# Kernel tuning notes

Hardware: AMD Instinct MI355X
Metric: run time of the kernel (lower is better)

The kernel has to match this reference:

```python
import jax, jax.numpy as jnp
import numpy as np

N_NODES = 50000
N_EDGES = 800000
D = 128


def setup_inputs() -> dict:
    key = jax.random.key(0)
    k1, k2, k3, k4 = jax.random.split(key, 4)
    x = jax.random.normal(k1, (N_NODES, D), dtype=jnp.float32)
    # nn.Linear(in, out, bias=False) weight: [out, in]
    W = jax.random.normal(k2, (D, D), dtype=jnp.float32) / np.sqrt(D)
    src = jax.random.randint(k3, (N_EDGES,), 0, N_NODES, dtype=jnp.int64)
    dst = jax.random.randint(k4, (N_EDGES,), 0, N_NODES, dtype=jnp.int64)
    return {"x": x, "W": W, "src": src, "dst": dst}


def reference(x, W, src, dst):
    # copy_src + reduce_sum: sum incoming neighbor features per destination node
    agg = jax.ops.segment_sum(x[src], dst, num_segments=N_NODES)  # [N, D]
    h = agg @ W.T                      # linear, no bias
    h = jax.nn.relu(h)                 # dropout is identity in eval mode
    h = h + x                          # residual (is_normalize=False)
    return h
```

## Files before the change

### kernel.cpp

```cpp
#include <hip/hip_runtime.h>

#define N_NODES 50000
#define N_EDGES 800000
#define D 128

#define P1_BLOCKS 128
#define P1_GRID   1024
#define EDGES_PER_BLOCK (N_EDGES / P1_BLOCKS)
#define N_BINS 782
#define CHUNK_CAP 31
#define CELL_WORDS 32
#define LIST_CAP 48
#define RS 136

#define WS_WB16   0
#define WS_SORTED 8192
#define WS_XBF16  3211264
#define WS_END_SORT ((size_t)(WS_XBF16 + 3200000) * 4)

#define NB_SCAN ((N_NODES + 255) / 256)
#define WS_CNT     0
#define WS_ROWPTR  50000
#define WS_BSUMS   100352
#define WS_SRCS    100608
#define WS_END_CSR ((size_t)(WS_SRCS + N_EDGES) * 4)

using bf16x8 = __attribute__((ext_vector_type(8))) short;
using f32x4  = __attribute__((ext_vector_type(4))) float;

__device__ __forceinline__ unsigned bf16rne(float f) {
    unsigned b = __float_as_uint(f);
    return (b + 0x7fffu + ((b >> 16) & 1u)) >> 16;
}

__device__ __forceinline__ uint4 pack8(float4 a, float4 b) {
    uint4 o;
    o.x = bf16rne(a.x) | (bf16rne(a.y) << 16);
    o.y = bf16rne(a.z) | (bf16rne(a.w) << 16);
    o.z = bf16rne(b.x) | (bf16rne(b.y) << 16);
    o.w = bf16rne(b.z) | (bf16rne(b.w) << 16);
    return o;
}

__global__ __launch_bounds__(256) void p1_convert_partition_kernel(
    const float* __restrict__ x, const float* __restrict__ W,
    const int* __restrict__ src, const int* __restrict__ dst,
    uint4* __restrict__ xb, uint4* __restrict__ wb,
    unsigned* __restrict__ sorted)
{
    const int tid = threadIdx.x;

    if (blockIdx.x >= P1_BLOCKS) {
        const int cb = blockIdx.x - P1_BLOCKS;
        const int gid = cb * 256 + tid;
        const int stride = (P1_GRID - P1_BLOCKS) * 256;
        const float4* x4 = (const float4*)x;
        for (int i = gid; i < (N_NODES * D) / 8; i += stride)
            xb[i] = pack8(x4[2 * i], x4[2 * i + 1]);
        const float4* W4 = (const float4*)W;
        for (int i = gid; i < (D * D) / 8; i += stride)
            wb[i] = pack8(W4[2 * i], W4[2 * i + 1]);
        return;
    }

    __shared__ int lhist[N_BINS];
    for (int b = tid; b < N_BINS; b += 256) lhist[b] = 0;
    __syncthreads();
    const int e0 = blockIdx.x * EDGES_PER_BLOCK;
    for (int i = tid; i < EDGES_PER_BLOCK; i += 256) {
        int e = e0 + i;
        int d = dst[e];
        int bin = d >> 6;
        int pos = atomicAdd(&lhist[bin], 1);
        if (pos < CHUNK_CAP)
            sorted[(size_t)(bin * P1_BLOCKS + blockIdx.x) * CELL_WORDS + 1 + pos] =
                ((unsigned)(d & 63) << 16) | ((unsigned)src[e] & 0xffffu);
    }
    __syncthreads();
    for (int b = tid; b < N_BINS; b += 256)
        sorted[(size_t)(b * P1_BLOCKS + blockIdx.x) * CELL_WORDS] = (unsigned)lhist[b];
}

__device__ __forceinline__ void acc_u4(float* acc, uint4 v)
{
    acc[0] += __uint_as_float(v.x << 16);
    acc[1] += __uint_as_float(v.x & 0xffff0000u);
    acc[2] += __uint_as_float(v.y << 16);
    acc[3] += __uint_as_float(v.y & 0xffff0000u);
    acc[4] += __uint_as_float(v.z << 16);
    acc[5] += __uint_as_float(v.z & 0xffff0000u);
    acc[6] += __uint_as_float(v.w << 16);
    acc[7] += __uint_as_float(v.w & 0xffff0000u);
}

__global__ __launch_bounds__(1024) void gather_gemm_kernel(
    const uint4* __restrict__ xb, const unsigned* __restrict__ sorted,
    const unsigned short* __restrict__ Wb, float* __restrict__ out)
{
    __shared__ unsigned short list[64 * LIST_CAP];
    __shared__ int lcnt[64];
    __shared__ unsigned short Ab[64 * RS];
    const int tid = threadIdx.x;
    const int bin = blockIdx.x;
    if (tid < 64) lcnt[tid] = 0;
    __syncthreads();

    {
        const int ch = tid >> 3;
        const int sub = tid & 7;
        const unsigned* base = sorted + (size_t)(bin * P1_BLOCKS + ch) * CELL_WORDS;
        int cc = (int)base[0];
        if (cc > CHUNK_CAP) cc = CHUNK_CAP;
        for (int i = sub; i < cc; i += 8) {
            unsigned p = base[1 + i];
            int dl = p >> 16;
            int pos = atomicAdd(&lcnt[dl], 1);
            if (pos < LIST_CAP) list[dl * LIST_CAP + pos] = (unsigned short)(p & 0xffffu);
        }
    }
    __syncthreads();

    {
        const int nl = tid >> 4;
        const int lane = tid & 15;
        int cc = lcnt[nl];
        if (cc > LIST_CAP) cc = LIST_CAP;
        const unsigned short* bk = &list[nl * LIST_CAP];

        float acc[8];
        #pragma unroll
        for (int i = 0; i < 8; ++i) acc[i] = 0.f;
        int e = 0;
        for (; e + 8 <= cc; e += 8) {
            uint4 v[8];
            #pragma unroll
            for (int j = 0; j < 8; ++j) v[j] = xb[(int)bk[e + j] * 16 + lane];
            #pragma unroll
            for (int j = 0; j < 8; ++j) acc_u4(acc, v[j]);
        }
        for (; e + 4 <= cc; e += 4) {
            uint4 v0 = xb[(int)bk[e] * 16 + lane];
            uint4 v1 = xb[(int)bk[e + 1] * 16 + lane];
            uint4 v2 = xb[(int)bk[e + 2] * 16 + lane];
            uint4 v3 = xb[(int)bk[e + 3] * 16 + lane];
            acc_u4(acc, v0); acc_u4(acc, v1); acc_u4(acc, v2); acc_u4(acc, v3);
        }
        for (; e < cc; ++e) acc_u4(acc, xb[(int)bk[e] * 16 + lane]);

        unsigned short* arow = &Ab[nl * RS + lane * 8];
        #pragma unroll
        for (int i = 0; i < 8; ++i) arow[i] = (unsigned short)bf16rne(acc[i]);
    }
    __syncthreads();

    const int wv = tid >> 6;
    const int lane64 = tid & 63;
    const int m = lane64 & 15;
    const int quad = lane64 >> 4;
    const int rt = wv >> 2;

    bf16x8 afrag[4];
    #pragma unroll
    for (int s = 0; s < 4; ++s)
        afrag[s] = *(const bf16x8*)(&Ab[(rt * 16 + m) * RS + quad * 8 + s * 32]);

    const unsigned short* xbs = (const unsigned short*)xb;

    #pragma unroll
    for (int half = 0; half < 2; ++half) {
        const int ct = (wv & 3) * 2 + half;
        f32x4 acc = {0.f, 0.f, 0.f, 0.f};
        const unsigned short* wrow = Wb + (size_t)(ct * 16 + m) * D + quad * 8;
        #pragma unroll
        for (int s = 0; s < 4; ++s) {
            bf16x8 bfrag = *(const bf16x8*)(wrow + s * 32);
            acc = __builtin_amdgcn_mfma_f32_16x16x32_bf16(afrag[s], bfrag, acc, 0, 0, 0);
        }
        const int cc2 = ct * 16 + m;
        #pragma unroll
        for (int r = 0; r < 4; ++r) {
            int rr = bin * 64 + rt * 16 + quad * 4 + r;
            if (rr < N_NODES) {
                float xf = __uint_as_float((unsigned)xbs[(size_t)rr * D + cc2] << 16);
                out[(size_t)rr * D + cc2] = fmaxf(acc[r], 0.f) + xf;
            }
        }
    }
}

__global__ __launch_bounds__(256) void hist_kernel(
    const int* __restrict__ dst, int* __restrict__ cnt)
{
    int e = blockIdx.x * 256 + threadIdx.x;
    if (e < N_EDGES) atomicAdd(&cnt[dst[e]], 1);
}

__device__ __forceinline__ int block_excl_scan_256(int v, int* wsums)
{
    const int lane = threadIdx.x & 63;
    const int wid = threadIdx.x >> 6;
    int incl = v;
    #pragma unroll
    for (int off = 1; off < 64; off <<= 1) {
        int t = __shfl_up(incl, off, 64);
        if (lane >= off) incl += t;
    }
    if (lane == 63) wsums[wid] = incl;
    __syncthreads();
    if (threadIdx.x == 0) {
        int s = 0;
        #pragma unroll
        for (int w = 0; w < 4; ++w) { int t = wsums[w]; wsums[w] = s; s += t; }
    }
    __syncthreads();
    return wsums[wid] + incl - v;
}

__global__ __launch_bounds__(256) void scan_reduce_kernel(
    const int* __restrict__ cnt, int* __restrict__ bsums)
{
    __shared__ int wsums[4];
    int i = blockIdx.x * 256 + threadIdx.x;
    int v = (i < N_NODES) ? cnt[i] : 0;
    const int lane = threadIdx.x & 63;
    int s = v;
    #pragma unroll
    for (int off = 32; off >= 1; off >>= 1) s += __shfl_down(s, off, 64);
    if (lane == 0) wsums[threadIdx.x >> 6] = s;
    __syncthreads();
    if (threadIdx.x == 0)
        bsums[blockIdx.x] = wsums[0] + wsums[1] + wsums[2] + wsums[3];
}

__global__ __launch_bounds__(256) void scan_bsums_kernel(
    int* __restrict__ bsums, int* __restrict__ row_ptr)
{
    __shared__ int wsums[4];
    int t = threadIdx.x;
    int v = (t < NB_SCAN) ? bsums[t] : 0;
    int excl = block_excl_scan_256(v, wsums);
    if (t < NB_SCAN) bsums[t] = excl;
    if (t == 255) row_ptr[N_NODES] = excl + v;
}

__global__ __launch_bounds__(256) void scan_final_kernel(
    int* __restrict__ cnt, const int* __restrict__ bsums,
    int* __restrict__ row_ptr)
{
    __shared__ int wsums[4];
    int i = blockIdx.x * 256 + threadIdx.x;
    int v = (i < N_NODES) ? cnt[i] : 0;
    int excl = block_excl_scan_256(v, wsums) + bsums[blockIdx.x];
    if (i < N_NODES) { row_ptr[i] = excl; cnt[i] = excl; }
}

__global__ __launch_bounds__(256) void csr_scatter_kernel(
    const int* __restrict__ src, const int* __restrict__ dst,
    int* __restrict__ cursor, int* __restrict__ srcs)
{
    int e = blockIdx.x * 256 + threadIdx.x;
    if (e < N_EDGES) {
        int pos = atomicAdd(&cursor[dst[e]], 1);
        srcs[pos] = src[e];
    }
}

__global__ __launch_bounds__(256) void gather_kernel(
    const float* __restrict__ x, const int* __restrict__ row_ptr,
    const int* __restrict__ srcs, float* __restrict__ agg)
{
    int gid = blockIdx.x * 256 + threadIdx.x;
    int node = gid >> 5;
    int lane = gid & 31;
    if (node >= N_NODES) return;
    int e = row_ptr[node];
    const int e_end = row_ptr[node + 1];
    const float4* x4 = (const float4*)x;
    float4 acc = make_float4(0.f, 0.f, 0.f, 0.f);
    for (; e + 4 <= e_end; e += 4) {
        int s0 = srcs[e], s1 = srcs[e + 1], s2 = srcs[e + 2], s3 = srcs[e + 3];
        float4 v0 = x4[(size_t)s0 * 32 + lane];
        float4 v1 = x4[(size_t)s1 * 32 + lane];
        float4 v2 = x4[(size_t)s2 * 32 + lane];
        float4 v3 = x4[(size_t)s3 * 32 + lane];
        acc.x += (v0.x + v1.x) + (v2.x + v3.x);
        acc.y += (v0.y + v1.y) + (v2.y + v3.y);
        acc.z += (v0.z + v1.z) + (v2.z + v3.z);
        acc.w += (v0.w + v1.w) + (v2.w + v3.w);
    }
    for (; e < e_end; ++e) {
        float4 v = x4[(size_t)srcs[e] * 32 + lane];
        acc.x += v.x; acc.y += v.y; acc.z += v.z; acc.w += v.w;
    }
    ((float4*)agg)[(size_t)node * 32 + lane] = acc;
}

__global__ __launch_bounds__(256) void scatter_add_kernel(
    const float* __restrict__ x, const int* __restrict__ src,
    const int* __restrict__ dst, float* __restrict__ agg)
{
    int gid = blockIdx.x * 256 + threadIdx.x;
    int edge = gid >> 5;
    int lane = gid & 31;
    if (edge >= N_EDGES) return;
    int s = src[edge];
    int d = dst[edge];
    const float4 v = *(const float4*)(x + (size_t)s * D + lane * 4);
    float* a = agg + (size_t)d * D + lane * 4;
    atomicAdd(a + 0, v.x);
    atomicAdd(a + 1, v.y);
    atomicAdd(a + 2, v.z);
    atomicAdd(a + 3, v.w);
}

#define G_ROWS 64

__global__ __launch_bounds__(256) void gemm_relu_res_kernel(
    float* __restrict__ agg, const float* __restrict__ W,
    const float* __restrict__ x)
{
    __shared__ float Wl[64 * 128];
    __shared__ float Al[G_ROWS * 128];

    const int tid = threadIdx.x;
    const int row0 = blockIdx.x * G_ROWS;

    for (int i = tid; i < G_ROWS * 32; i += 256) {
        int r = i >> 5;
        int c4 = (i & 31) << 2;
        int gr = row0 + r;
        float4 v = make_float4(0.f, 0.f, 0.f, 0.f);
        if (gr < N_NODES) v = *(const float4*)(agg + (size_t)gr * D + c4);
        *(float4*)(Al + r * 128 + c4) = v;
    }

    const int cg = tid & 31;
    const int rg = tid >> 5;
    const int c0 = cg << 2;
    const int r0 = rg << 3;

    float acc[8][4];
    #pragma unroll
    for (int i = 0; i < 8; ++i)
        #pragma unroll
        for (int j = 0; j < 4; ++j) acc[i][j] = 0.f;

    for (int h = 0; h < 2; ++h) {
        __syncthreads();
        for (int i = tid; i < 64 * 128; i += 256) {
            int c = i >> 6, kk = i & 63;
            int c_swz = (((c >> 2) ^ (kk & 31)) << 2) | (c & 3);
            Wl[kk * 128 + c_swz] = W[c * 128 + h * 64 + kk];
        }
        __syncthreads();

        for (int kc = 0; kc < 64; kc += 4) {
            float a[8][4];
            #pragma unroll
            for (int i = 0; i < 8; ++i) {
                float4 t = *(const float4*)(&Al[(r0 + i) * 128 + h * 64 + kc]);
                a[i][0] = t.x; a[i][1] = t.y; a[i][2] = t.z; a[i][3] = t.w;
            }
            #pragma unroll
            for (int j = 0; j < 4; ++j) {
                int kk = kc + j;
                const float4 wv =
                    *(const float4*)(&Wl[kk * 128 + ((cg ^ (kk & 31)) << 2)]);
                #pragma unroll
                for (int i = 0; i < 8; ++i) {
                    acc[i][0] = fmaf(a[i][j], wv.x, acc[i][0]);
                    acc[i][1] = fmaf(a[i][j], wv.y, acc[i][1]);
                    acc[i][2] = fmaf(a[i][j], wv.z, acc[i][2]);
                    acc[i][3] = fmaf(a[i][j], wv.w, acc[i][3]);
                }
            }
        }
    }

    #pragma unroll
    for (int i = 0; i < 8; ++i) {
        int gr = row0 + r0 + i;
        if (gr >= N_NODES) continue;
        const float4 xv = *(const float4*)(x + (size_t)gr * D + c0);
        float4 o;
        o.x = fmaxf(acc[i][0], 0.f) + xv.x;
        o.y = fmaxf(acc[i][1], 0.f) + xv.y;
        o.z = fmaxf(acc[i][2], 0.f) + xv.z;
        o.w = fmaxf(acc[i][3], 0.f) + xv.w;
        *(float4*)(agg + (size_t)gr * D + c0) = o;
    }
}

extern "C" void kernel_launch(void* const* d_in, const int* in_sizes, int n_in,
                              void* d_out, int out_size, void* d_ws, size_t ws_size,
                              hipStream_t stream) {
    const float* x  = (const float*)d_in[0];
    const float* W  = (const float*)d_in[1];
    const int*  src = (const int*)d_in[2];
    const int*  dst = (const int*)d_in[3];
    float* agg = (float*)d_out;

    const int eb = (N_EDGES + 255) / 256;
    int* ws = (int*)d_ws;

    if (ws_size >= WS_END_SORT) {
        uint4*    wb     = (uint4*)(ws + WS_WB16);
        unsigned* sorted = (unsigned*)(ws + WS_SORTED);
        uint4*    xb     = (uint4*)(ws + WS_XBF16);

        p1_convert_partition_kernel<<<P1_GRID, 256, 0, stream>>>(
            x, W, src, dst, xb, wb, sorted);
        gather_gemm_kernel<<<N_BINS, 1024, 0, stream>>>(
            xb, sorted, (const unsigned short*)wb, (float*)d_out);
    } else if (ws_size >= WS_END_CSR) {
        int* cnt     = ws + WS_CNT;
        int* row_ptr = ws + WS_ROWPTR;
        int* bsums   = ws + WS_BSUMS;
        int* srcs    = ws + WS_SRCS;

        hipMemsetAsync(cnt, 0, (size_t)N_NODES * sizeof(int), stream);
        hist_kernel<<<eb, 256, 0, stream>>>(dst, cnt);
        scan_reduce_kernel<<<NB_SCAN, 256, 0, stream>>>(cnt, bsums);
        scan_bsums_kernel<<<1, 256, 0, stream>>>(bsums, row_ptr);
        scan_final_kernel<<<NB_SCAN, 256, 0, stream>>>(cnt, bsums, row_ptr);
        csr_scatter_kernel<<<eb, 256, 0, stream>>>(src, dst, cnt, srcs);
        int total = N_NODES * 32;
        gather_kernel<<<(total + 255) / 256, 256, 0, stream>>>(x, row_ptr, srcs, agg);
        gemm_relu_res_kernel<<<(N_NODES + G_ROWS - 1) / G_ROWS, 256, 0, stream>>>(agg, W, x);
    } else {
        hipMemsetAsync(agg, 0, (size_t)N_NODES * D * sizeof(float), stream);
        int total = N_EDGES * 32;
        scatter_add_kernel<<<(total + 255) / 256, 256, 0, stream>>>(x, src, dst, agg);
        gemm_relu_res_kernel<<<(N_NODES + G_ROWS - 1) / G_ROWS, 256, 0, stream>>>(agg, W, x);
    }
}
```

Measured before the change: 159.7 us.

## Fuse partition/convert and gather-GEMM into one cooperative kernel with grid sync

Combines the edge-partition/bf16-conversion kernel and the gather+MFMA GEMM kernel into a single cooperative launch of 512 blocks of 1024 threads. A grid-wide sync separates the phases, and the second phase loops over bins with a grid stride. The aim is to remove the second kernel launch and the inter-kernel gap. In exchange, each phase runs on fewer threads than before (128 partition blocks at 1024 threads, and 512 blocks for 782 bins, so some blocks handle two bins). A grid sync is added, and if the cooperative launch fails the code falls back to the old two-kernel path.

```diff
diff --git a/kernel.cpp b/kernel.cpp
--- a/kernel.cpp
+++ b/kernel.cpp
@@ -1,4 +1,7 @@
 #include <hip/hip_runtime.h>
+#include <hip/hip_cooperative_groups.h>
+
+namespace cg = cooperative_groups;
 
 #define N_NODES 50000
 #define N_EDGES 800000
@@ -6,6 +9,7 @@
 
 #define P1_BLOCKS 128
 #define P1_GRID   1024
+#define FUSED_GRID 512
 #define EDGES_PER_BLOCK (N_EDGES / P1_BLOCKS)
 #define N_BINS 782
 #define CHUNK_CAP 31
@@ -40,6 +44,150 @@
     o.z = bf16rne(b.x) | (bf16rne(b.y) << 16);
     o.w = bf16rne(b.z) | (bf16rne(b.w) << 16);
     return o;
+}
+
+__device__ __forceinline__ void acc_u4(float* acc, uint4 v)
+{
+    acc[0] += __uint_as_float(v.x << 16);
+    acc[1] += __uint_as_float(v.x & 0xffff0000u);
+    acc[2] += __uint_as_float(v.y << 16);
+    acc[3] += __uint_as_float(v.y & 0xffff0000u);
+    acc[4] += __uint_as_float(v.z << 16);
+    acc[5] += __uint_as_float(v.z & 0xffff0000u);
+    acc[6] += __uint_as_float(v.w << 16);
+    acc[7] += __uint_as_float(v.w & 0xffff0000u);
+}
+
+__global__ __launch_bounds__(1024, 8) void fused_gcn_kernel(
+    const float* __restrict__ x, const float* __restrict__ W,
+    const int* __restrict__ src, const int* __restrict__ dst,
+    uint4* __restrict__ xb, uint4* __restrict__ wb,
+    unsigned* __restrict__ sorted, float* __restrict__ out)
+{
+    __shared__ int lhist[N_BINS];
+    __shared__ unsigned short list[64 * LIST_CAP];
+    __shared__ int lcnt[64];
+    __shared__ unsigned short Ab[64 * RS];
+    const int tid = threadIdx.x;
+    const int bid = blockIdx.x;
+
+    if (bid < P1_BLOCKS) {
+        for (int b = tid; b < N_BINS; b += 1024) lhist[b] = 0;
+        __syncthreads();
+        const int e0 = bid * EDGES_PER_BLOCK;
+        for (int i = tid; i < EDGES_PER_BLOCK; i += 1024) {
+            int e = e0 + i;
+            int d = dst[e];
+            int bin = d >> 6;
+            int pos = atomicAdd(&lhist[bin], 1);
+            if (pos < CHUNK_CAP)
+                sorted[(size_t)(bin * P1_BLOCKS + bid) * CELL_WORDS + 1 + pos] =
+                    ((unsigned)(d & 63) << 16) | ((unsigned)src[e] & 0xffffu);
+        }
+        __syncthreads();
+        for (int b = tid; b < N_BINS; b += 1024)
+            sorted[(size_t)(b * P1_BLOCKS + bid) * CELL_WORDS] = (unsigned)lhist[b];
+    } else {
+        const int gid = (bid - P1_BLOCKS) * 1024 + tid;
+        const int stride = (FUSED_GRID - P1_BLOCKS) * 1024;
+        const float4* x4 = (const float4*)x;
+        for (int i = gid; i < (N_NODES * D) / 8; i += stride)
+            xb[i] = pack8(x4[2 * i], x4[2 * i + 1]);
+        const float4* W4 = (const float4*)W;
+        for (int i = gid; i < (D * D) / 8; i += stride)
+            wb[i] = pack8(W4[2 * i], W4[2 * i + 1]);
+    }
+
+    __threadfence();
+    cg::this_grid().sync();
+
+    const unsigned short* Wb  = (const unsigned short*)wb;
+    const unsigned short* xbs = (const unsigned short*)xb;
+
+    for (int bin = bid; bin < N_BINS; bin += FUSED_GRID) {
+        if (tid < 64) lcnt[tid] = 0;
+        __syncthreads();
+
+        {
+            const int ch = tid >> 3;
+            const int sub = tid & 7;
+            const unsigned* base = sorted + (size_t)(bin * P1_BLOCKS + ch) * CELL_WORDS;
+            int cc = (int)base[0];
+            if (cc > CHUNK_CAP) cc = CHUNK_CAP;
+            for (int i = sub; i < cc; i += 8) {
+                unsigned p = base[1 + i];
+                int dl = p >> 16;
+                int pos = atomicAdd(&lcnt[dl], 1);
+                if (pos < LIST_CAP) list[dl * LIST_CAP + pos] = (unsigned short)(p & 0xffffu);
+            }
+        }
+        __syncthreads();
+
+        {
+            const int nl = tid >> 4;
+            const int lane = tid & 15;
+            int cc = lcnt[nl];
+            if (cc > LIST_CAP) cc = LIST_CAP;
+            const unsigned short* bk = &list[nl * LIST_CAP];
+
+            float acc[8];
+            #pragma unroll
+            for (int i = 0; i < 8; ++i) acc[i] = 0.f;
+            int e = 0;
+            for (; e + 8 <= cc; e += 8) {
+                uint4 v[8];
+                #pragma unroll
+                for (int j = 0; j < 8; ++j) v[j] = xb[(int)bk[e + j] * 16 + lane];
+                #pragma unroll
+                for (int j = 0; j < 8; ++j) acc_u4(acc, v[j]);
+            }
+            for (; e + 4 <= cc; e += 4) {
+                uint4 v0 = xb[(int)bk[e] * 16 + lane];
+                uint4 v1 = xb[(int)bk[e + 1] * 16 + lane];
+                uint4 v2 = xb[(int)bk[e + 2] * 16 + lane];
+                uint4 v3 = xb[(int)bk[e + 3] * 16 + lane];
+                acc_u4(acc, v0); acc_u4(acc, v1); acc_u4(acc, v2); acc_u4(acc, v3);
+            }
+            for (; e < cc; ++e) acc_u4(acc, xb[(int)bk[e] * 16 + lane]);
+
+            unsigned short* arow = &Ab[nl * RS + lane * 8];
+            #pragma unroll
+            for (int i = 0; i < 8; ++i) arow[i] = (unsigned short)bf16rne(acc[i]);
+        }
+        __syncthreads();
+
+        const int wv = tid >> 6;
+        const int lane64 = tid & 63;
+        const int m = lane64 & 15;
+        const int quad = lane64 >> 4;
+        const int rt = wv >> 2;
+
+        bf16x8 afrag[4];
+        #pragma unroll
+        for (int s = 0; s < 4; ++s)
+            afrag[s] = *(const bf16x8*)(&Ab[(rt * 16 + m) * RS + quad * 8 + s * 32]);
+
+        #pragma unroll
+        for (int half = 0; half < 2; ++half) {
+            const int ct = (wv & 3) * 2 + half;
+            f32x4 acc = {0.f, 0.f, 0.f, 0.f};
+            const unsigned short* wrow = Wb + (size_t)(ct * 16 + m) * D + quad * 8;
+            #pragma unroll
+            for (int s = 0; s < 4; ++s) {
+                bf16x8 bfrag = *(const bf16x8*)(wrow + s * 32);
+                acc = __builtin_amdgcn_mfma_f32_16x16x32_bf16(afrag[s], bfrag, acc, 0, 0, 0);
+            }
+            const int cc2 = ct * 16 + m;
+            #pragma unroll
+            for (int r = 0; r < 4; ++r) {
+                int rr = bin * 64 + rt * 16 + quad * 4 + r;
+                if (rr < N_NODES) {
+                    float xf = __uint_as_float((unsigned)xbs[(size_t)rr * D + cc2] << 16);
+                    out[(size_t)rr * D + cc2] = fmaxf(acc[r], 0.f) + xf;
+                }
+            }
+        }
+    }
 }
 
 __global__ __launch_bounds__(256) void p1_convert_partition_kernel(
@@ -79,18 +227,6 @@
     __syncthreads();
     for (int b = tid; b < N_BINS; b += 256)
         sorted[(size_t)(b * P1_BLOCKS + blockIdx.x) * CELL_WORDS] = (unsigned)lhist[b];
-}
-
-__device__ __forceinline__ void acc_u4(float* acc, uint4 v)
-{
-    acc[0] += __uint_as_float(v.x << 16);
-    acc[1] += __uint_as_float(v.x & 0xffff0000u);
-    acc[2] += __uint_as_float(v.y << 16);
-    acc[3] += __uint_as_float(v.y & 0xffff0000u);
-    acc[4] += __uint_as_float(v.z << 16);
-    acc[5] += __uint_as_float(v.z & 0xffff0000u);
-    acc[6] += __uint_as_float(v.w << 16);
-    acc[7] += __uint_as_float(v.w & 0xffff0000u);
 }
 
 __global__ __launch_bounds__(1024) void gather_gemm_kernel(
@@ -407,11 +543,19 @@
         uint4*    wb     = (uint4*)(ws + WS_WB16);
         unsigned* sorted = (unsigned*)(ws + WS_SORTED);
         uint4*    xb     = (uint4*)(ws + WS_XBF16);
-
-        p1_convert_partition_kernel<<<P1_GRID, 256, 0, stream>>>(
-            x, W, src, dst, xb, wb, sorted);
-        gather_gemm_kernel<<<N_BINS, 1024, 0, stream>>>(
-            xb, sorted, (const unsigned short*)wb, (float*)d_out);
+        float*    out    = (float*)d_out;
+
+        void* args[] = { (void*)&x, (void*)&W, (void*)&src, (void*)&dst,
+                         (void*)&xb, (void*)&wb, (void*)&sorted, (void*)&out };
+        hipError_t err = hipLaunchCooperativeKernel(
+            (const void*)fused_gcn_kernel, dim3(FUSED_GRID), dim3(1024),
+            args, 0, stream);
+        if (err != hipSuccess) {
+            p1_convert_partition_kernel<<<P1_GRID, 256, 0, stream>>>(
+                x, W, src, dst, xb, wb, sorted);
+            gather_gemm_kernel<<<N_BINS, 1024, 0, stream>>>(
+                xb, sorted, (const unsigned short*)wb, out);
+        }
     } else if (ws_size >= WS_END_CSR) {
         int* cnt     = ws + WS_CNT;
         int* row_ptr = ws + WS_ROWPTR;
```

Result: slower. 496.2 us (+210.8%).
